# Optimization experiments

Hardware: AMD Instinct MI355X
Metric: run time of the kernel (lower is better)

The kernel has to match this reference:

```python
import jax, jax.numpy as jnp
import numpy as np

B, T, D, H = 8, 4096, 1024, 1024

def setup_inputs() -> dict:
    key = jax.random.key(0)
    k1, k2, k3, k4, k5 = jax.random.split(key, 5)
    s = 1.0 / np.sqrt(D)  # nn.Linear default init scale
    return {
        "x": jax.random.normal(k1, (B, T, D), dtype=jnp.float32),
        "Wz": jax.random.uniform(k2, (H, D), dtype=jnp.float32, minval=-s, maxval=s),
        "bz": jax.random.uniform(k3, (H,), dtype=jnp.float32, minval=-s, maxval=s),
        "Wh": jax.random.uniform(k4, (H, D), dtype=jnp.float32, minval=-s, maxval=s),
        "bh": jax.random.uniform(k5, (H,), dtype=jnp.float32, minval=-s, maxval=s),
    }

def log_g(x):
    # Appendix B.3 of 'Were RNNs All We Needed?'
    return jnp.where(x >= 0, jnp.log(jax.nn.relu(x) + 0.5), -jax.nn.softplus(-x))

def reference(x, Wz, bz, Wh, bh):
    # Linear projections: [B,T,D] @ [D,H] -> [B,T,H]
    k = jnp.einsum('btd,hd->bth', x, Wz) + bz
    tilde_h = jnp.einsum('btd,hd->bth', x, Wh) + bh
    log_z = -jax.nn.softplus(-k)           # log sigmoid(k)
    log_one_minus_z = -jax.nn.softplus(k)  # log (1 - sigmoid(k))
    log_tilde_h = log_g(tilde_h)
    # parallel scan in log space: h[i] = a[i]*h[i-1] + b[i]
    log_a_star = jnp.cumsum(log_one_minus_z, axis=1)
    log_x = log_a_star + jax.lax.cumlogsumexp(log_z + log_tilde_h - log_a_star, axis=1)
    return jnp.exp(log_x)
```

## Files before the change

kernel.cpp:

```cpp
#include <hip/hip_runtime.h>
#include <cstdint>

typedef unsigned short u16;
typedef __attribute__((ext_vector_type(8))) __bf16 bf16x8_t;
typedef __attribute__((ext_vector_type(4))) float f32x4_t;
typedef __attribute__((ext_vector_type(4))) uint32_t u32x4_t;

constexpr int Bn = 8, Tn = 4096, Dn = 1024, Hn = 1024;
constexpr int Mn = Bn * Tn;
constexpr int NC = 128, CL = Tn / NC;

__device__ __forceinline__ u16 f2bf(float f) {
  uint32_t u = __builtin_bit_cast(uint32_t, f);
  u += 0x7FFFu + ((u >> 16) & 1u);
  return (u16)(u >> 16);
}

__global__ __launch_bounds__(256) void cvt_all(
    const float* __restrict__ x, const float* __restrict__ wz, const float* __restrict__ wh,
    u16* __restrict__ xb, u16* __restrict__ wzb, u16* __restrict__ whb) {
  int i = blockIdx.x * 256 + threadIdx.x;
  const float* s; u16* d; int off;
  if (i < 8388608)      { s = x;  d = xb;  off = i; }
  else if (i < 8650752) { s = wz; d = wzb; off = i - 8388608; }
  else                  { s = wh; d = whb; off = i - 8650752; }
  f32x4_t v = __builtin_nontemporal_load(&((const f32x4_t*)s)[off]);
  ushort4 o;
  o.x = f2bf(v.x); o.y = f2bf(v.y); o.z = f2bf(v.z); o.w = f2bf(v.w);
  ((ushort4*)d)[off] = o;
}

__device__ __forceinline__ void gl_lds16(const void* g, void* l) {
  __builtin_amdgcn_global_load_lds((const __attribute__((address_space(1))) void*)g,
                                   (__attribute__((address_space(3))) void*)l, 16u, 0, 0u);
}

__device__ __forceinline__ void gates(float kv, float tv, float& a, float& bb) {
  float e  = __expf(-kv);
  float rc = __builtin_amdgcn_rcpf(1.f + e);
  a = e * rc;
  float g = (tv >= 0.f) ? (tv + 0.5f)
                        : __builtin_amdgcn_rcpf(1.f + __expf(-tv));
  bb = rc * g;
}

__global__ __launch_bounds__(256) void gemm_fused(
    const u16* __restrict__ A, const u16* __restrict__ Wz, const u16* __restrict__ Wh,
    const float* __restrict__ bz, const float* __restrict__ bh,
    uint32_t* __restrict__ gAB, float* __restrict__ Aagg, float* __restrict__ Bagg) {
  constexpr int K = 1024;
  const uint bid = blockIdx.x;
  const uint xcd = bid & 7;
  const uint seq = bid >> 3;
  const uint ht  = seq & 15;
  const uint mt  = (seq >> 4) * 8 + xcd;
  const int m0 = mt * 128;
  const int h0 = ht * 64;

  __shared__ u16 lA [2][128 * 32];
  __shared__ u16 lBz[2][64 * 32];
  __shared__ u16 lBh[2][64 * 32];

  const int tid  = threadIdx.x;
  const int lane = tid & 63;
  const int wave = tid >> 6;
  const int wm   = wave >> 1;
  const int wh   = wave & 1;

  const int csA = (((lane & 3) ^ ((lane >> 3) & 3)) * 8);
  const int csB = (((tid  & 3) ^ ((tid  >> 3) & 3)) * 8);
  const u16* gA0 = A  + (size_t)(m0 + wave * 16 + (lane >> 2)) * K + csA;
  const u16* gBz = Wz + (size_t)(h0 + (tid >> 2)) * K + csB;
  const u16* gBh = Wh + (size_t)(h0 + (tid >> 2)) * K + csB;
  const int woff = wave * 512;

  const int fr   = lane & 15;
  const int KB   = lane >> 4;
  const int fcol = (KB ^ ((fr >> 1) & 3)) * 8;

  f32x4_t az[4][2] = {}, ah[4][2] = {};

  for (int kt = 0; kt < K; kt += 64) {
    gl_lds16(gA0 + kt,                         lA[0] + woff);
    gl_lds16(gA0 + kt + (size_t)64 * K,        lA[0] + woff + 2048);
    gl_lds16(gA0 + kt + 32,                    lA[1] + woff);
    gl_lds16(gA0 + kt + 32 + (size_t)64 * K,   lA[1] + woff + 2048);
    gl_lds16(gBz + kt,                         lBz[0] + woff);
    gl_lds16(gBz + kt + 32,                    lBz[1] + woff);
    gl_lds16(gBh + kt,                         lBh[0] + woff);
    gl_lds16(gBh + kt + 32,                    lBh[1] + woff);
    __syncthreads();
#pragma unroll
    for (int half = 0; half < 2; ++half) {
      bf16x8_t af[4], bzf[2], bhf[2];
#pragma unroll
      for (int i = 0; i < 4; ++i)
        af[i] = *(const bf16x8_t*)&lA[half][(wm * 64 + i * 16 + fr) * 32 + fcol];
#pragma unroll
      for (int j = 0; j < 2; ++j) {
        bzf[j] = *(const bf16x8_t*)&lBz[half][(wh * 32 + j * 16 + fr) * 32 + fcol];
        bhf[j] = *(const bf16x8_t*)&lBh[half][(wh * 32 + j * 16 + fr) * 32 + fcol];
      }
#pragma unroll
      for (int i = 0; i < 4; ++i)
#pragma unroll
        for (int j = 0; j < 2; ++j) {
          az[i][j] = __builtin_amdgcn_mfma_f32_16x16x32_bf16(af[i], bzf[j], az[i][j], 0, 0, 0);
          ah[i][j] = __builtin_amdgcn_mfma_f32_16x16x32_bf16(af[i], bhf[j], ah[i][j], 0, 0, 0);
        }
    }
    __syncthreads();
  }

  const int cr = (lane >> 4) * 4;
  const int cc = lane & 15;
  const int b  = mt >> 5;

#pragma unroll
  for (int j = 0; j < 2; ++j) {
    float bvz = bz[h0 + wh * 32 + j * 16 + cc];
    float bvh = bh[h0 + wh * 32 + j * 16 + cc];
#pragma unroll
    for (int cp = 0; cp < 2; ++cp) {
      float Ai[2], Bi[2];
#pragma unroll
      for (int i2 = 0; i2 < 2; ++i2) {
        const int i = cp * 2 + i2;
        float Al = 1.f, Bl = 0.f;
#pragma unroll
        for (int r = 0; r < 4; ++r) {
          float kv = az[i][j][r] + bvz;
          float tv = ah[i][j][r] + bvh;
          float a, bb;
          gates(kv, tv, a, bb);
          _Float16 a16 = (_Float16)a, b16 = (_Float16)bb;
          uint32_t pk = (uint32_t)__builtin_bit_cast(u16, a16) |
                        ((uint32_t)__builtin_bit_cast(u16, b16) << 16);
          __builtin_nontemporal_store(
              pk, &gAB[(size_t)(m0 + wm * 64 + i * 16 + cr + r) * Hn +
                       h0 + wh * 32 + j * 16 + cc]);
          float ar = (float)a16, br = (float)b16;
          Al = Al * ar;
          Bl = fmaf(ar, Bl, br);
        }
        float Ahi = __shfl_down(Al, 16), Bhi = __shfl_down(Bl, 16);
        float A2 = Ahi * Al;
        float B2 = fmaf(Ahi, Bl, Bhi);
        Ahi = __shfl_down(A2, 32); Bhi = __shfl_down(B2, 32);
        Ai[i2] = Ahi * A2;
        Bi[i2] = fmaf(Ahi, B2, Bhi);
      }
      float Aw = Ai[1] * Ai[0];
      float Bw = fmaf(Ai[1], Bi[0], Bi[1]);
      if (lane < 16) {
        const int tc = (mt & 31) * 4 + wm * 2 + cp;
        size_t ai = ((size_t)(b * NC + tc)) * Hn + h0 + wh * 32 + j * 16 + lane;
        Aagg[ai] = Aw;
        Bagg[ai] = Bw;
      }
    }
  }
}

__global__ __launch_bounds__(64) void scan_phase_b(
    const float* Aagg, const float* __restrict__ Bagg, float* carry) {
  int h = blockIdx.x * 64 + threadIdx.x;
  int b = blockIdx.y;
  const size_t base = (size_t)b * NC * Hn + h;
  float state = 0.f;
  constexpr int PF = 16;
  float Av[PF], Bv[PF];
  for (int g = 0; g < NC; g += PF) {
#pragma unroll
    for (int u = 0; u < PF; ++u) {
      size_t idx = base + (size_t)(g + u) * Hn;
      Av[u] = Aagg[idx];
      Bv[u] = Bagg[idx];
    }
#pragma unroll
    for (int u = 0; u < PF; ++u) {
      size_t idx = base + (size_t)(g + u) * Hn;
      carry[idx] = state;
      state = fmaf(Av[u], state, Bv[u]);
    }
  }
}

__global__ __launch_bounds__(256) void scan_phase_c(
    const uint32_t* __restrict__ gAB, const float* __restrict__ carry,
    float* __restrict__ out) {
  int h0 = threadIdx.x * 4;
  int c = blockIdx.x, b = blockIdx.y;
  f32x4_t hst = *(const f32x4_t*)(carry + ((size_t)(b * NC + c)) * Hn + h0);
  size_t base = ((size_t)b * Tn + (size_t)c * CL) * Hn + h0;
#pragma unroll 4
  for (int t = 0; t < CL; ++t) {
    size_t idx = base + (size_t)t * Hn;
    u32x4_t v = __builtin_nontemporal_load((const u32x4_t*)(gAB + idx));
    uint32_t vv[4] = {v.x, v.y, v.z, v.w};
#pragma unroll
    for (int u = 0; u < 4; ++u) {
      float a = (float)__builtin_bit_cast(_Float16, (u16)(vv[u] & 0xFFFFu));
      float bb = (float)__builtin_bit_cast(_Float16, (u16)(vv[u] >> 16));
      hst[u] = fmaf(a, hst[u], bb);
    }
    __builtin_nontemporal_store(hst, (f32x4_t*)(out + idx));
  }
}

extern "C" void kernel_launch(void* const* d_in, const int* in_sizes, int n_in,
                              void* d_out, int out_size, void* d_ws, size_t ws_size,
                              hipStream_t stream) {
  const float* x  = (const float*)d_in[0];
  const float* Wz = (const float*)d_in[1];
  const float* bz = (const float*)d_in[2];
  const float* Wh = (const float*)d_in[3];
  const float* bh = (const float*)d_in[4];
  float* out = (float*)d_out;

  char* ws = (char*)d_ws;
  u16*      xbf   = (u16*)     (ws);
  u16*      wzbf  = (u16*)     (ws + 67108864);
  u16*      whbf  = (u16*)     (ws + 69206016);
  uint32_t* gAB   = (uint32_t*)(ws + 71303168);
  float*    Aagg  = (float*)   (ws + 205520896);
  float*    Bagg  = (float*)   (ws + 209715200);
  float*    carry = Aagg;

  cvt_all<<<dim3(34816), 256, 0, stream>>>(x, Wz, Wh, xbf, wzbf, whbf);
  gemm_fused<<<dim3(4096), 256, 0, stream>>>(xbf, wzbf, whbf, bz, bh, gAB, Aagg, Bagg);
  scan_phase_b<<<dim3(16, Bn), 64, 0, stream>>>(Aagg, Bagg, carry);
  scan_phase_c<<<dim3(NC, Bn), 256, 0, stream>>>(gAB, carry, out);
}
```

Measured before the change: 439.8 us.

## Double-buffer GEMM K-loop with prefetch of next 32-wide slice

Restructures the fused GEMM main loop from a load-all-then-compute 64-wide K step into a 32-wide ping-pong pipeline. The next K slice is issued via global_load_lds into the alternate LDS buffer before computing on the current one, and a partial vmcnt wait lets loads overlap MFMA work. This is meant to hide global memory latency that the previous fully synchronous loop exposed. The trade-off is twice as many barriers per K and reliance on hand-written waitcnt counts matching the number of outstanding loads.

```diff
diff --git a/kernel.cpp b/kernel.cpp
--- a/kernel.cpp
+++ b/kernel.cpp
@@ -80,36 +80,43 @@
 
   f32x4_t az[4][2] = {}, ah[4][2] = {};
 
-  for (int kt = 0; kt < K; kt += 64) {
-    gl_lds16(gA0 + kt,                         lA[0] + woff);
-    gl_lds16(gA0 + kt + (size_t)64 * K,        lA[0] + woff + 2048);
-    gl_lds16(gA0 + kt + 32,                    lA[1] + woff);
-    gl_lds16(gA0 + kt + 32 + (size_t)64 * K,   lA[1] + woff + 2048);
-    gl_lds16(gBz + kt,                         lBz[0] + woff);
-    gl_lds16(gBz + kt + 32,                    lBz[1] + woff);
-    gl_lds16(gBh + kt,                         lBh[0] + woff);
-    gl_lds16(gBh + kt + 32,                    lBh[1] + woff);
-    __syncthreads();
-#pragma unroll
-    for (int half = 0; half < 2; ++half) {
-      bf16x8_t af[4], bzf[2], bhf[2];
-#pragma unroll
-      for (int i = 0; i < 4; ++i)
-        af[i] = *(const bf16x8_t*)&lA[half][(wm * 64 + i * 16 + fr) * 32 + fcol];
+  gl_lds16(gA0,                  lA[0] + woff);
+  gl_lds16(gA0 + (size_t)64 * K, lA[0] + woff + 2048);
+  gl_lds16(gBz,                  lBz[0] + woff);
+  gl_lds16(gBh,                  lBh[0] + woff);
+
+#pragma unroll 2
+  for (int kt = 0; kt < K; kt += 32) {
+    const int cur = (kt >> 5) & 1;
+    const int nxt = cur ^ 1;
+    if (kt + 32 < K) {
+      gl_lds16(gA0 + kt + 32,                  lA[nxt] + woff);
+      gl_lds16(gA0 + kt + 32 + (size_t)64 * K, lA[nxt] + woff + 2048);
+      gl_lds16(gBz + kt + 32,                  lBz[nxt] + woff);
+      gl_lds16(gBh + kt + 32,                  lBh[nxt] + woff);
+      asm volatile("s_waitcnt vmcnt(4)" ::: "memory");
+    } else {
+      asm volatile("s_waitcnt vmcnt(0)" ::: "memory");
+    }
+    __builtin_amdgcn_s_barrier();
+
+    bf16x8_t af[4], bzf[2], bhf[2];
+#pragma unroll
+    for (int i = 0; i < 4; ++i)
+      af[i] = *(const bf16x8_t*)&lA[cur][(wm * 64 + i * 16 + fr) * 32 + fcol];
+#pragma unroll
+    for (int j = 0; j < 2; ++j) {
+      bzf[j] = *(const bf16x8_t*)&lBz[cur][(wh * 32 + j * 16 + fr) * 32 + fcol];
+      bhf[j] = *(const bf16x8_t*)&lBh[cur][(wh * 32 + j * 16 + fr) * 32 + fcol];
+    }
+#pragma unroll
+    for (int i = 0; i < 4; ++i)
 #pragma unroll
       for (int j = 0; j < 2; ++j) {
-        bzf[j] = *(const bf16x8_t*)&lBz[half][(wh * 32 + j * 16 + fr) * 32 + fcol];
-        bhf[j] = *(const bf16x8_t*)&lBh[half][(wh * 32 + j * 16 + fr) * 32 + fcol];
+        az[i][j] = __builtin_amdgcn_mfma_f32_16x16x32_bf16(af[i], bzf[j], az[i][j], 0, 0, 0);
+        ah[i][j] = __builtin_amdgcn_mfma_f32_16x16x32_bf16(af[i], bhf[j], ah[i][j], 0, 0, 0);
       }
-#pragma unroll
-      for (int i = 0; i < 4; ++i)
-#pragma unroll
-        for (int j = 0; j < 2; ++j) {
-          az[i][j] = __builtin_amdgcn_mfma_f32_16x16x32_bf16(af[i], bzf[j], az[i][j], 0, 0, 0);
-          ah[i][j] = __builtin_amdgcn_mfma_f32_16x16x32_bf16(af[i], bhf[j], ah[i][j], 0, 0, 0);
-        }
-    }
-    __syncthreads();
+    __builtin_amdgcn_s_barrier();
   }
 
   const int cr = (lane >> 4) * 4;
```

New measurement: 451.3 us. 1.03x slower.
